# Kernel optimization log

Measured on AMD Instinct MI355X. Metric: run time of the kernel, lower is better.

Reference implementation:

```python
import jax, jax.numpy as jnp
import numpy as np

N_TOKENS = 16384
MODEL_DIM = 2048
NUM_EXPERTS = 64
K = 2


def setup_inputs() -> dict:
    key = jax.random.key(0)
    k1, k2 = jax.random.split(key)
    inputs = jax.random.normal(k1, (N_TOKENS, MODEL_DIM), dtype=jnp.float32)
    # gate weight, torch Linear(model_dim, num_experts, bias=False) -> [E, D]
    wg_weight = jax.random.normal(k2, (NUM_EXPERTS, MODEL_DIM), dtype=jnp.float32) * 0.02
    return {"inputs": inputs, "wg_weight": wg_weight}


def reference(inputs, wg_weight):
    E = wg_weight.shape[0]
    # gate computed in fp32 (module casts input and keeps wg in float32)
    logits = jnp.einsum("nd,ed->ne", inputs.astype(jnp.float32), wg_weight)
    probs = jax.nn.softmax(logits, axis=-1)                      # [N, E]
    topk_probs, topk_indices = jax.lax.top_k(probs, K)           # [N, K]
    flat_idx = topk_indices.reshape(-1)                          # [N*K]
    # stable sort of expert ids over all (token, slot) pairs
    sort_ordering = jnp.argsort(flat_idx)                        # [N*K]
    # reverse permutation: reversed[sort_ordering[i]] = i
    ar = jnp.arange(flat_idx.shape[0], dtype=sort_ordering.dtype)
    reversed_ordering = jnp.zeros_like(sort_ordering).at[sort_ordering].set(ar)
    # map slot index back to token index
    token_order = sort_ordering // K
    # per-expert counts (== unique_consecutive counts scattered into [E])
    input_splits = jnp.bincount(flat_idx, length=E).astype(jnp.int64)
    # combine weights: renormalize top-k probs via softmax when k > 1
    if K > 1:
        combine_weights = jax.nn.softmax(topk_probs, axis=-1)
    else:
        combine_weights = topk_probs
    combine_weights = combine_weights.reshape(-1).astype(inputs.dtype)
    return token_order, reversed_ordering, combine_weights, input_splits, probs
```

## Files before the change

### kernel.cpp

```cpp
#include <hip/hip_runtime.h>
#include <math.h>

#define N_TOKENS    16384
#define MODEL_DIM   2048
#define NUM_EXPERTS 64
#define NK          (N_TOKENS * 2)

#define OFF_TOKEN_ORDER 0
#define OFF_REVERSED    (NK)
#define OFF_COMBINE     (2 * NK)
#define OFF_SPLITS      (3 * NK)
#define OFF_PROBS       (3 * NK + NUM_EXPERTS)

#define NSEG 256
#define NFRAG 16384

#define B_BYTES  16384
#define A_BYTES  8192
#define STAGE_BYTES (B_BYTES + A_BYTES)

typedef _Float16 half8 __attribute__((ext_vector_type(8)));
typedef float    f32x4 __attribute__((ext_vector_type(4)));

#define MEMFENCE asm volatile("" ::: "memory")

__device__ __forceinline__ void glds16(const void* g, void* l) {
    __builtin_amdgcn_global_load_lds(
        (const __attribute__((address_space(1))) void*)g,
        (__attribute__((address_space(3))) void*)l, 16, 0, 0);
}

__global__ __launch_bounds__(256) void preconvert(
    const float* __restrict__ w, half8* __restrict__ WH, half8* __restrict__ WL,
    int* __restrict__ segHist)
{
    const int fr = blockIdx.x * 256 + threadIdx.x;
    const int lane = fr & 63;
    const int tile = (fr >> 6) & 3;
    const int kstep = fr >> 8;
    const int e = tile * 16 + (lane & 15);
    const int kb = kstep * 32 + (lane >> 4) * 8;
    const float* src = w + (size_t)e * MODEL_DIM + kb;
    const float4 w0 = *(const float4*)(src);
    const float4 w1 = *(const float4*)(src + 4);
    const float av[8] = {w0.x, w0.y, w0.z, w0.w, w1.x, w1.y, w1.z, w1.w};
    half8 hh, hl;
#pragma unroll
    for (int j = 0; j < 8; j++) {
        const float v = av[j] * 64.0f;
        const _Float16 h = (_Float16)v;
        hh[j] = h;
        hl[j] = (_Float16)((v - (float)h) * 4096.0f);
    }
    WH[fr] = hh;
    WL[fr] = hl;
    segHist[fr] = 0;
}

__global__ __launch_bounds__(256, 2) void gate_fused(
    const float* __restrict__ x, const half8* __restrict__ WH,
    const half8* __restrict__ WL, float* __restrict__ out,
    int* __restrict__ flat_idx, int* __restrict__ segHist)
{
    __shared__ alignas(16) unsigned char smem[2 * STAGE_BYTES];

    const int tid  = threadIdx.x;
    const int wv   = tid >> 6;
    const int lane = tid & 63;
    const int kh   = wv & 1;
    const int tg   = wv >> 1;
    const int t0   = blockIdx.x * 32;
    const int col  = lane & 15;
    const int kg   = lane >> 4;

    const unsigned char* s_ptr[6];
    int s_stride[6];
    int s_off[6];
#pragma unroll
    for (int i = 0; i < 6; i++) {
        const int c = wv * 6 + i;
        if (c < 16) {
            const int hl   = c & 1;
            const int tile = (c >> 1) & 3;
            const int ckh  = c >> 3;
            const half8* base = (hl ? WL : WH) + ((size_t)((ckh * 32) * 4 + tile) * 64 + lane);
            s_ptr[i]    = (const unsigned char*)base;
            s_stride[i] = 4096;
            s_off[i]    = c * 1024 + lane * 16;
        } else {
            const int a   = c - 16;
            const int cc  = a & 1;
            const int ctg = (a >> 1) & 1;
            const int ckh = a >> 2;
            const float* base = x + (size_t)(t0 + ctg * 16 + (lane & 15)) * MODEL_DIM
                              + ckh * 1024 + (lane >> 4) * 8 + cc * 4;
            s_ptr[i]    = (const unsigned char*)base;
            s_stride[i] = 128;
            s_off[i]    = B_BYTES + a * 1024 + lane * 16;
        }
    }

    f32x4 accH[4], accC[4];
    double accD[4][4];
#pragma unroll
    for (int t = 0; t < 4; t++) {
        accH[t] = (f32x4){0.f, 0.f, 0.f, 0.f};
        accC[t] = (f32x4){0.f, 0.f, 0.f, 0.f};
#pragma unroll
        for (int r = 0; r < 4; r++) accD[t][r] = 0.0;
    }

#pragma unroll
    for (int i = 0; i < 6; i++) glds16(s_ptr[i], smem + s_off[i]);

    const int aoff = B_BYTES + (kh * 4 + tg * 2) * 1024 + lane * 16;
    const int boff = (kh * 4) * 2048 + lane * 16;

    for (int j = 0; j < 32; j++) {
        const int jn = (j < 31) ? j + 1 : 31;
        unsigned char* nbuf = smem + ((j + 1) & 1) * STAGE_BYTES;
#pragma unroll
        for (int i = 0; i < 6; i++)
            glds16(s_ptr[i] + (size_t)jn * s_stride[i], nbuf + s_off[i]);

        asm volatile("s_waitcnt vmcnt(6)" ::: "memory");
        __builtin_amdgcn_s_barrier();
        MEMFENCE;

        const unsigned char* buf = smem + (j & 1) * STAGE_BYTES;

        const float4 a0 = *(const float4*)(buf + aoff);
        const float4 a1 = *(const float4*)(buf + aoff + 1024);
        const float av[8] = {a0.x, a0.y, a0.z, a0.w, a1.x, a1.y, a1.z, a1.w};
        half8 ah, al;
#pragma unroll
        for (int q = 0; q < 8; q++) {
            const float v = av[q];
            const _Float16 h = (_Float16)v;
            ah[q] = h;
            al[q] = (_Float16)((v - (float)h) * 4096.0f);
        }

#pragma unroll
        for (int t = 0; t < 4; t++) {
            const half8 bh = *(const half8*)(buf + boff + t * 2048);
            const half8 bl = *(const half8*)(buf + boff + t * 2048 + 1024);
            accH[t] = __builtin_amdgcn_mfma_f32_16x16x32_f16(ah, bh, accH[t], 0, 0, 0);
            accC[t] = __builtin_amdgcn_mfma_f32_16x16x32_f16(ah, bl, accC[t], 0, 0, 0);
            accC[t] = __builtin_amdgcn_mfma_f32_16x16x32_f16(al, bh, accC[t], 0, 0, 0);
        }

        if ((j & 7) == 7) {
#pragma unroll
            for (int t = 0; t < 4; t++)
#pragma unroll
                for (int r = 0; r < 4; r++) {
                    accD[t][r] += (double)accH[t][r] + (double)accC[t][r] * (1.0 / 4096.0);
                    accH[t][r] = 0.0f;
                    accC[t][r] = 0.0f;
                }
        }

        MEMFENCE;
        __builtin_amdgcn_s_barrier();
    }

    asm volatile("s_waitcnt vmcnt(0)" ::: "memory");
    __syncthreads();

    double* red = (double*)smem;
    if (kh == 1) {
#pragma unroll
        for (int t = 0; t < 4; t++)
#pragma unroll
            for (int r = 0; r < 4; r++)
                red[(tg * 64 + lane) * 17 + t * 4 + r] = accD[t][r];
    }
    __syncthreads();
    if (kh == 1) return;

#pragma unroll
    for (int t = 0; t < 4; t++)
#pragma unroll
        for (int r = 0; r < 4; r++)
            accD[t][r] += red[(tg * 64 + lane) * 17 + t * 4 + r];

    const int rowg = lane >> 4;
#pragma unroll
    for (int r = 0; r < 4; r++) {
        float lv[4];
#pragma unroll
        for (int t = 0; t < 4; t++) lv[t] = (float)(accD[t][r] * (1.0 / 64.0));

        float m = fmaxf(fmaxf(lv[0], lv[1]), fmaxf(lv[2], lv[3]));
#pragma unroll
        for (int d = 1; d < 16; d <<= 1) m = fmaxf(m, __shfl_xor(m, d));

        float l1 = -INFINITY, l2 = -INFINITY;
        int i1 = 0, i2 = 0;
#pragma unroll
        for (int t = 0; t < 4; t++) {
            const float l = lv[t];
            const int e = t * 16 + col;
            if (l > l1)      { l2 = l1; i2 = i1; l1 = l; i1 = e; }
            else if (l > l2) { l2 = l;  i2 = e; }
        }
#pragma unroll
        for (int d = 1; d < 16; d <<= 1) {
            const float ol1 = __shfl_xor(l1, d), ol2 = __shfl_xor(l2, d);
            const int   oi1 = __shfl_xor(i1, d), oi2 = __shfl_xor(i2, d);
            if (ol1 > l1 || (ol1 == l1 && oi1 < i1)) {
                if (l1 > ol2 || (l1 == ol2 && i1 < oi2)) { l2 = l1;  i2 = i1;  }
                else                                     { l2 = ol2; i2 = oi2; }
                l1 = ol1; i1 = oi1;
            } else if (ol1 > l2 || (ol1 == l2 && oi1 < i2)) {
                l2 = ol1; i2 = oi1;
            }
        }

        float ex[4];
        double sd = 0.0;
#pragma unroll
        for (int t = 0; t < 4; t++) { ex[t] = expf(lv[t] - m); sd += (double)ex[t]; }
#pragma unroll
        for (int d = 1; d < 16; d <<= 1) sd += __shfl_xor(sd, d);
        const float inv = (float)(1.0 / sd);

        const int tok = t0 + tg * 16 + rowg * 4 + r;
        float* pp = out + OFF_PROBS + (size_t)tok * NUM_EXPERTS + col;
#pragma unroll
        for (int t = 0; t < 4; t++) pp[t * 16] = ex[t] * inv;

        if (col == 0) {
            const float p1 = expf(l1 - m) * inv;
            const float p2 = expf(l2 - m) * inv;
            const float e2 = expf(p2 - p1);
            const float rr = 1.0f / (1.0f + e2);
            out[OFF_COMBINE + 2 * tok]     = rr;
            out[OFF_COMBINE + 2 * tok + 1] = e2 * rr;
            flat_idx[2 * tok]     = i1;
            flat_idx[2 * tok + 1] = i2;
            atomicAdd(&segHist[(tok >> 6) * NUM_EXPERTS + i1], 1);
            atomicAdd(&segHist[(tok >> 6) * NUM_EXPERTS + i2], 1);
        }
    }
}

__global__ __launch_bounds__(256) void scan_kernel(
    const int* __restrict__ segHist, int* __restrict__ segOff,
    float* __restrict__ out)
{
    __shared__ int h[NSEG * NUM_EXPERTS];
    __shared__ int gtot[4 * NUM_EXPERTS];
    __shared__ int base[NUM_EXPERTS];
    const int tid = threadIdx.x;
    for (int i = tid; i < NSEG * NUM_EXPERTS / 4; i += 256)
        *(int4*)(h + i * 4) = *(const int4*)(segHist + i * 4);
    __syncthreads();

    const int e = tid & 63;
    const int g = tid >> 6;
    int run = 0;
    for (int s = g * 64; s < g * 64 + 64; s++) {
        const int idx = s * NUM_EXPERTS + e;
        const int v = h[idx];
        h[idx] = run;
        run += v;
    }
    gtot[g * NUM_EXPERTS + e] = run;
    __syncthreads();

    if (tid < NUM_EXPERTS) {
        int b = 0;
#pragma unroll
        for (int gg = 0; gg < 4; gg++) {
            const int t = gtot[gg * NUM_EXPERTS + tid];
            gtot[gg * NUM_EXPERTS + tid] = b;
            b += t;
        }
        out[OFF_SPLITS + tid] = (float)b;
        int xs = b;
#pragma unroll
        for (int off = 1; off < 64; off <<= 1) {
            const int v = __shfl_up(xs, off);
            if (tid >= off) xs += v;
        }
        base[tid] = xs - b;
    }
    __syncthreads();

    const int myoff = gtot[g * NUM_EXPERTS + e] + base[e];
    for (int s = g * 64; s < g * 64 + 64; s++) {
        const int idx = s * NUM_EXPERTS + e;
        segOff[idx] = h[idx] + myoff;
    }
}

__global__ __launch_bounds__(256) void scatter_kernel(
    const int* __restrict__ flat_idx, const int* __restrict__ segOff,
    float* __restrict__ out)
{
    __shared__ int cnt[2 * NUM_EXPERTS];
    const int tid = threadIdx.x;
    const int i = blockIdx.x * 256 + tid;
    const int e = flat_idx[i];
    const int lane = tid & 63;
    const int wv = tid >> 6;
    const int segslot = wv >> 1;
    const int seg = i >> 7;

    if (tid < 2 * NUM_EXPERTS) cnt[tid] = 0;
    __syncthreads();

    unsigned long long match = ~0ull;
#pragma unroll
    for (int b = 0; b < 6; b++) {
        const unsigned long long m = __ballot((e >> b) & 1);
        match &= ((e >> b) & 1) ? m : ~m;
    }
    const int rank = __popcll(match & ((1ull << lane) - 1ull));

    int pos = 0;
    if ((wv & 1) == 0) {
        pos = segOff[seg * NUM_EXPERTS + e] + rank;
        if (lane == __builtin_ctzll(match))
            cnt[segslot * NUM_EXPERTS + e] = __popcll(match);
    }
    __syncthreads();
    if ((wv & 1) == 1)
        pos = segOff[seg * NUM_EXPERTS + e] + cnt[segslot * NUM_EXPERTS + e] + rank;

    out[OFF_TOKEN_ORDER + pos] = (float)(i >> 1);
    out[OFF_REVERSED + i]      = (float)pos;
}

extern "C" void kernel_launch(void* const* d_in, const int* in_sizes, int n_in,
                              void* d_out, int out_size, void* d_ws, size_t ws_size,
                              hipStream_t stream) {
    const float* x = (const float*)d_in[0];
    const float* w = (const float*)d_in[1];
    float* out = (float*)d_out;

    int* flat_idx = (int*)d_ws;
    int* segHist  = flat_idx + NK;
    int* segOff   = segHist + NSEG * NUM_EXPERTS;
    half8* WH = (half8*)(segOff + NSEG * NUM_EXPERTS);
    half8* WL = WH + NFRAG;

    preconvert<<<64, 256, 0, stream>>>(w, WH, WL, segHist);
    gate_fused<<<512, 256, 0, stream>>>(x, WH, WL, out, flat_idx, segHist);
    scan_kernel<<<1, 256, 0, stream>>>(segHist, segOff, out);
    scatter_kernel<<<NK / 256, 256, 0, stream>>>(flat_idx, segOff, out);
}
```

Baseline: 224.8 us.

## Triple-buffer global-to-LDS loads and swizzle activation tile layout

Moves the gate GEMM main loop from double to triple buffering, prefetching two stages ahead with vmcnt(12), so more global-memory latency is hidden. It also remaps which wave issues which chunk, interleaving the chunks across waves. The activation tile is reloaded with a row-per-8-lanes XOR-swizzled layout to give longer contiguous reads per token and fewer LDS bank conflicts. LDS per block grows by half, which may cut occupancy below the two blocks per CU requested.

```diff
diff --git a/kernel.cpp b/kernel.cpp
--- a/kernel.cpp
+++ b/kernel.cpp
@@ -62,7 +62,7 @@
     const half8* __restrict__ WL, float* __restrict__ out,
     int* __restrict__ flat_idx, int* __restrict__ segHist)
 {
-    __shared__ alignas(16) unsigned char smem[2 * STAGE_BYTES];
+    __shared__ alignas(16) unsigned char smem[3 * STAGE_BYTES];
 
     const int tid  = threadIdx.x;
     const int wv   = tid >> 6;
@@ -78,23 +78,23 @@
     int s_off[6];
 #pragma unroll
     for (int i = 0; i < 6; i++) {
-        const int c = wv * 6 + i;
+        const int c = i * 4 + wv;
         if (c < 16) {
             const int hl   = c & 1;
             const int tile = (c >> 1) & 3;
             const int ckh  = c >> 3;
-            const half8* base = (hl ? WL : WH) + ((size_t)((ckh * 32) * 4 + tile) * 64 + lane);
+            const half8* base = (hl ? WL : WH) + ((size_t)(ckh * 32 * 4 + tile) * 64 + lane);
             s_ptr[i]    = (const unsigned char*)base;
             s_stride[i] = 4096;
             s_off[i]    = c * 1024 + lane * 16;
         } else {
             const int a   = c - 16;
-            const int cc  = a & 1;
-            const int ctg = (a >> 1) & 1;
             const int ckh = a >> 2;
-            const float* base = x + (size_t)(t0 + ctg * 16 + (lane & 15)) * MODEL_DIM
-                              + ckh * 1024 + (lane >> 4) * 8 + cc * 4;
-            s_ptr[i]    = (const unsigned char*)base;
+            const int tgp = a & 3;
+            const int tok = t0 + tgp * 8 + (lane >> 3);
+            const int p   = (lane & 7) ^ (lane >> 3);
+            s_ptr[i]    = (const unsigned char*)(x + (size_t)tok * MODEL_DIM
+                                                 + ckh * 1024 + p * 4);
             s_stride[i] = 128;
             s_off[i]    = B_BYTES + a * 1024 + lane * 16;
         }
@@ -112,25 +112,35 @@
 
 #pragma unroll
     for (int i = 0; i < 6; i++) glds16(s_ptr[i], smem + s_off[i]);
-
-    const int aoff = B_BYTES + (kh * 4 + tg * 2) * 1024 + lane * 16;
-    const int boff = (kh * 4) * 2048 + lane * 16;
+#pragma unroll
+    for (int i = 0; i < 6; i++)
+        glds16(s_ptr[i] + s_stride[i], smem + STAGE_BYTES + s_off[i]);
+
+    const int a_r   = kh * 4 + tg * 2 + (col >> 3);
+    const int tl    = col & 7;
+    const int abase = B_BYTES + a_r * 1024 + tl * 128;
+    const int aoff0 = abase + (((kg * 2) ^ tl) << 4);
+    const int aoff1 = abase + (((kg * 2 + 1) ^ tl) << 4);
+    const int boff  = kh * 8192 + lane * 16;
+
+    int cur = 0;
+    int nxt = 2;
 
     for (int j = 0; j < 32; j++) {
-        const int jn = (j < 31) ? j + 1 : 31;
-        unsigned char* nbuf = smem + ((j + 1) & 1) * STAGE_BYTES;
+        const int jn = (j < 30) ? j + 2 : 31;
+        unsigned char* nbuf = smem + nxt * STAGE_BYTES;
 #pragma unroll
         for (int i = 0; i < 6; i++)
             glds16(s_ptr[i] + (size_t)jn * s_stride[i], nbuf + s_off[i]);
 
-        asm volatile("s_waitcnt vmcnt(6)" ::: "memory");
+        asm volatile("s_waitcnt vmcnt(12)" ::: "memory");
         __builtin_amdgcn_s_barrier();
         MEMFENCE;
 
-        const unsigned char* buf = smem + (j & 1) * STAGE_BYTES;
-
-        const float4 a0 = *(const float4*)(buf + aoff);
-        const float4 a1 = *(const float4*)(buf + aoff + 1024);
+        const unsigned char* buf = smem + cur * STAGE_BYTES;
+
+        const float4 a0 = *(const float4*)(buf + aoff0);
+        const float4 a1 = *(const float4*)(buf + aoff1);
         const float av[8] = {a0.x, a0.y, a0.z, a0.w, a1.x, a1.y, a1.z, a1.w};
         half8 ah, al;
 #pragma unroll
@@ -163,6 +173,9 @@
 
         MEMFENCE;
         __builtin_amdgcn_s_barrier();
+
+        cur = (cur == 2) ? 0 : cur + 1;
+        nxt = (nxt == 2) ? 0 : nxt + 1;
     }
 
     asm volatile("s_waitcnt vmcnt(0)" ::: "memory");
```

Result: no change. 224.2 us (-0.3%).

## Per-wave A staging with register-prefetched B and fuse scan into scatter

Applied to the files above, without the earlier changes.

The GEMM main loop drops the block-wide double-buffered LDS stage and its two barriers per step. Each wave now streams its own A tile through a swizzled triple buffer in LDS and prefetches the preconverted B fragments straight into registers, ping-ponging between two register sets. Separately, the single-block scan kernel is merged into the scatter kernel: every scatter block recomputes the full prefix scan from segHist in shared memory, which removes one launch and the segOff round trip. The cost is that the scan work is repeated in all 128 blocks, and the loop carries more register pressure.

```diff
diff --git a/kernel.cpp b/kernel.cpp
--- a/kernel.cpp
+++ b/kernel.cpp
@@ -15,14 +15,8 @@
 #define NSEG 256
 #define NFRAG 16384
 
-#define B_BYTES  16384
-#define A_BYTES  8192
-#define STAGE_BYTES (B_BYTES + A_BYTES)
-
 typedef _Float16 half8 __attribute__((ext_vector_type(8)));
 typedef float    f32x4 __attribute__((ext_vector_type(4)));
-
-#define MEMFENCE asm volatile("" ::: "memory")
 
 __device__ __forceinline__ void glds16(const void* g, void* l) {
     __builtin_amdgcn_global_load_lds(
@@ -62,7 +56,8 @@
     const half8* __restrict__ WL, float* __restrict__ out,
     int* __restrict__ flat_idx, int* __restrict__ segHist)
 {
-    __shared__ alignas(16) unsigned char smem[2 * STAGE_BYTES];
+    __shared__ alignas(16) unsigned char astage[4][3][2048];
+    __shared__ double red[128 * 17];
 
     const int tid  = threadIdx.x;
     const int wv   = tid >> 6;
@@ -73,32 +68,19 @@
     const int col  = lane & 15;
     const int kg   = lane >> 4;
 
-    const unsigned char* s_ptr[6];
-    int s_stride[6];
-    int s_off[6];
-#pragma unroll
-    for (int i = 0; i < 6; i++) {
-        const int c = wv * 6 + i;
-        if (c < 16) {
-            const int hl   = c & 1;
-            const int tile = (c >> 1) & 3;
-            const int ckh  = c >> 3;
-            const half8* base = (hl ? WL : WH) + ((size_t)((ckh * 32) * 4 + tile) * 64 + lane);
-            s_ptr[i]    = (const unsigned char*)base;
-            s_stride[i] = 4096;
-            s_off[i]    = c * 1024 + lane * 16;
-        } else {
-            const int a   = c - 16;
-            const int cc  = a & 1;
-            const int ctg = (a >> 1) & 1;
-            const int ckh = a >> 2;
-            const float* base = x + (size_t)(t0 + ctg * 16 + (lane & 15)) * MODEL_DIM
-                              + ckh * 1024 + (lane >> 4) * 8 + cc * 4;
-            s_ptr[i]    = (const unsigned char*)base;
-            s_stride[i] = 128;
-            s_off[i]    = B_BYTES + a * 1024 + lane * 16;
-        }
-    }
+    const int r3 = lane >> 3;
+    const int pp = (lane & 7) ^ r3;
+    const float* pA0 = x + (size_t)(t0 + tg * 16 + r3) * MODEL_DIM + kh * 1024 + pp * 4;
+    const float* pA1 = x + (size_t)(t0 + tg * 16 + 8 + r3) * MODEL_DIM + kh * 1024 + pp * 4;
+    unsigned char* mys = &astage[wv][0][0];
+
+    const int rr  = col & 7;
+    const int rb  = (col >> 3) * 1024 + rr * 128;
+    const int ro0 = rb + (((2 * kg)     ^ rr) << 4);
+    const int ro1 = rb + (((2 * kg + 1) ^ rr) << 4);
+
+    const half8* pbh = WH + ((size_t)kh * 32 * 4) * 64 + lane;
+    const half8* pbl = WL + ((size_t)kh * 32 * 4) * 64 + lane;
 
     f32x4 accH[4], accC[4];
     double accD[4][4];
@@ -110,65 +92,75 @@
         for (int r = 0; r < 4; r++) accD[t][r] = 0.0;
     }
 
-#pragma unroll
-    for (int i = 0; i < 6; i++) glds16(s_ptr[i], smem + s_off[i]);
-
-    const int aoff = B_BYTES + (kh * 4 + tg * 2) * 1024 + lane * 16;
-    const int boff = (kh * 4) * 2048 + lane * 16;
-
-    for (int j = 0; j < 32; j++) {
-        const int jn = (j < 31) ? j + 1 : 31;
-        unsigned char* nbuf = smem + ((j + 1) & 1) * STAGE_BYTES;
-#pragma unroll
-        for (int i = 0; i < 6; i++)
-            glds16(s_ptr[i] + (size_t)jn * s_stride[i], nbuf + s_off[i]);
-
-        asm volatile("s_waitcnt vmcnt(6)" ::: "memory");
-        __builtin_amdgcn_s_barrier();
-        MEMFENCE;
-
-        const unsigned char* buf = smem + (j & 1) * STAGE_BYTES;
-
-        const float4 a0 = *(const float4*)(buf + aoff);
-        const float4 a1 = *(const float4*)(buf + aoff + 1024);
-        const float av[8] = {a0.x, a0.y, a0.z, a0.w, a1.x, a1.y, a1.z, a1.w};
-        half8 ah, al;
-#pragma unroll
-        for (int q = 0; q < 8; q++) {
-            const float v = av[q];
-            const _Float16 h = (_Float16)v;
-            ah[q] = h;
-            al[q] = (_Float16)((v - (float)h) * 4096.0f);
-        }
-
-#pragma unroll
-        for (int t = 0; t < 4; t++) {
-            const half8 bh = *(const half8*)(buf + boff + t * 2048);
-            const half8 bl = *(const half8*)(buf + boff + t * 2048 + 1024);
-            accH[t] = __builtin_amdgcn_mfma_f32_16x16x32_f16(ah, bh, accH[t], 0, 0, 0);
-            accC[t] = __builtin_amdgcn_mfma_f32_16x16x32_f16(ah, bl, accC[t], 0, 0, 0);
-            accC[t] = __builtin_amdgcn_mfma_f32_16x16x32_f16(al, bh, accC[t], 0, 0, 0);
-        }
-
-        if ((j & 7) == 7) {
-#pragma unroll
-            for (int t = 0; t < 4; t++)
-#pragma unroll
-                for (int r = 0; r < 4; r++) {
-                    accD[t][r] += (double)accH[t][r] + (double)accC[t][r] * (1.0 / 4096.0);
-                    accH[t][r] = 0.0f;
-                    accC[t][r] = 0.0f;
-                }
-        }
-
-        MEMFENCE;
-        __builtin_amdgcn_s_barrier();
-    }
+    half8 bhA[4], blA[4], bhB[4], blB[4];
+
+    glds16(pA0, mys);
+    glds16(pA1, mys + 1024);
+    glds16(pA0 + 32, mys + 2048);
+    glds16(pA1 + 32, mys + 2048 + 1024);
+#pragma unroll
+    for (int t = 0; t < 4; t++) {
+        bhA[t] = pbh[t * 64];
+        blA[t] = pbl[t * 64];
+    }
+
+    int j = 0, curb = 0, dstb = 2;
+
+#define BODY(BHC, BLC, BHN, BLN) do {                                        \
+    const int jn2 = (j < 30) ? (j + 2) : 31;                                 \
+    glds16(pA0 + jn2 * 32, mys + dstb * 2048);                               \
+    glds16(pA1 + jn2 * 32, mys + dstb * 2048 + 1024);                        \
+    const half8* pbh_n = pbh + ((j < 31) ? 256 : 0);                         \
+    const half8* pbl_n = pbl + ((j < 31) ? 256 : 0);                         \
+    _Pragma("unroll")                                                        \
+    for (int t_ = 0; t_ < 4; t_++) {                                         \
+        BHN[t_] = pbh_n[t_ * 64];                                            \
+        BLN[t_] = pbl_n[t_ * 64];                                            \
+    }                                                                        \
+    pbh = pbh_n; pbl = pbl_n;                                                \
+    asm volatile("s_waitcnt vmcnt(10)" ::: "memory");                        \
+    __builtin_amdgcn_sched_barrier(0);                                       \
+    const float4 a0 = *(const float4*)(mys + curb * 2048 + ro0);             \
+    const float4 a1 = *(const float4*)(mys + curb * 2048 + ro1);             \
+    const float av_[8] = {a0.x, a0.y, a0.z, a0.w, a1.x, a1.y, a1.z, a1.w};   \
+    half8 ah, al;                                                            \
+    _Pragma("unroll")                                                        \
+    for (int q_ = 0; q_ < 8; q_++) {                                         \
+        const float v_ = av_[q_];                                            \
+        const _Float16 h_ = (_Float16)v_;                                    \
+        ah[q_] = h_;                                                         \
+        al[q_] = (_Float16)((v_ - (float)h_) * 4096.0f);                     \
+    }                                                                        \
+    _Pragma("unroll")                                                        \
+    for (int t_ = 0; t_ < 4; t_++) {                                         \
+        accH[t_] = __builtin_amdgcn_mfma_f32_16x16x32_f16(ah, BHC[t_], accH[t_], 0, 0, 0); \
+        accC[t_] = __builtin_amdgcn_mfma_f32_16x16x32_f16(ah, BLC[t_], accC[t_], 0, 0, 0); \
+        accC[t_] = __builtin_amdgcn_mfma_f32_16x16x32_f16(al, BHC[t_], accC[t_], 0, 0, 0); \
+    }                                                                        \
+    if ((j & 7) == 7) {                                                      \
+        _Pragma("unroll")                                                    \
+        for (int t_ = 0; t_ < 4; t_++)                                       \
+        _Pragma("unroll")                                                    \
+        for (int r_ = 0; r_ < 4; r_++) {                                     \
+            accD[t_][r_] += (double)accH[t_][r_] + (double)accC[t_][r_] * (1.0 / 4096.0); \
+            accH[t_][r_] = 0.0f;                                             \
+            accC[t_][r_] = 0.0f;                                             \
+        }                                                                    \
+    }                                                                        \
+    curb = (curb == 2) ? 0 : curb + 1;                                       \
+    dstb = (dstb == 2) ? 0 : dstb + 1;                                       \
+    j++;                                                                     \
+} while (0)
+
+    for (int jj = 0; jj < 16; jj++) {
+        BODY(bhA, blA, bhB, blB);
+        BODY(bhB, blB, bhA, blA);
+    }
+#undef BODY
 
     asm volatile("s_waitcnt vmcnt(0)" ::: "memory");
     __syncthreads();
 
-    double* red = (double*)smem;
     if (kh == 1) {
 #pragma unroll
         for (int t = 0; t < 4; t++)
@@ -227,17 +219,17 @@
         const float inv = (float)(1.0 / sd);
 
         const int tok = t0 + tg * 16 + rowg * 4 + r;
-        float* pp = out + OFF_PROBS + (size_t)tok * NUM_EXPERTS + col;
-#pragma unroll
-        for (int t = 0; t < 4; t++) pp[t * 16] = ex[t] * inv;
+        float* pp2 = out + OFF_PROBS + (size_t)tok * NUM_EXPERTS + col;
+#pragma unroll
+        for (int t = 0; t < 4; t++) pp2[t * 16] = ex[t] * inv;
 
         if (col == 0) {
             const float p1 = expf(l1 - m) * inv;
             const float p2 = expf(l2 - m) * inv;
             const float e2 = expf(p2 - p1);
-            const float rr = 1.0f / (1.0f + e2);
-            out[OFF_COMBINE + 2 * tok]     = rr;
-            out[OFF_COMBINE + 2 * tok + 1] = e2 * rr;
+            const float rr2 = 1.0f / (1.0f + e2);
+            out[OFF_COMBINE + 2 * tok]     = rr2;
+            out[OFF_COMBINE + 2 * tok + 1] = e2 * rr2;
             flat_idx[2 * tok]     = i1;
             flat_idx[2 * tok + 1] = i2;
             atomicAdd(&segHist[(tok >> 6) * NUM_EXPERTS + i1], 1);
@@ -246,16 +238,19 @@
     }
 }
 
-__global__ __launch_bounds__(256) void scan_kernel(
-    const int* __restrict__ segHist, int* __restrict__ segOff,
+__global__ __launch_bounds__(256) void scan_scatter(
+    const int* __restrict__ flat_idx, const int* __restrict__ segHist,
     float* __restrict__ out)
 {
     __shared__ int h[NSEG * NUM_EXPERTS];
     __shared__ int gtot[4 * NUM_EXPERTS];
-    __shared__ int base[NUM_EXPERTS];
+    __shared__ int base_[NUM_EXPERTS];
+    __shared__ int cnt[2 * NUM_EXPERTS];
+
     const int tid = threadIdx.x;
     for (int i = tid; i < NSEG * NUM_EXPERTS / 4; i += 256)
         *(int4*)(h + i * 4) = *(const int4*)(segHist + i * 4);
+    if (tid < 2 * NUM_EXPERTS) cnt[tid] = 0;
     __syncthreads();
 
     const int e = tid & 63;
@@ -278,57 +273,44 @@
             gtot[gg * NUM_EXPERTS + tid] = b;
             b += t;
         }
-        out[OFF_SPLITS + tid] = (float)b;
+        if (blockIdx.x == 0) out[OFF_SPLITS + tid] = (float)b;
         int xs = b;
 #pragma unroll
         for (int off = 1; off < 64; off <<= 1) {
             const int v = __shfl_up(xs, off);
             if (tid >= off) xs += v;
         }
-        base[tid] = xs - b;
-    }
-    __syncthreads();
-
-    const int myoff = gtot[g * NUM_EXPERTS + e] + base[e];
-    for (int s = g * 64; s < g * 64 + 64; s++) {
-        const int idx = s * NUM_EXPERTS + e;
-        segOff[idx] = h[idx] + myoff;
-    }
-}
-
-__global__ __launch_bounds__(256) void scatter_kernel(
-    const int* __restrict__ flat_idx, const int* __restrict__ segOff,
-    float* __restrict__ out)
-{
-    __shared__ int cnt[2 * NUM_EXPERTS];
-    const int tid = threadIdx.x;
+        base_[tid] = xs - b;
+    }
+    __syncthreads();
+
     const int i = blockIdx.x * 256 + tid;
-    const int e = flat_idx[i];
+    const int ee = flat_idx[i];
     const int lane = tid & 63;
     const int wv = tid >> 6;
     const int segslot = wv >> 1;
     const int seg = i >> 7;
 
-    if (tid < 2 * NUM_EXPERTS) cnt[tid] = 0;
-    __syncthreads();
-
     unsigned long long match = ~0ull;
 #pragma unroll
     for (int b = 0; b < 6; b++) {
-        const unsigned long long m = __ballot((e >> b) & 1);
-        match &= ((e >> b) & 1) ? m : ~m;
+        const unsigned long long m = __ballot((ee >> b) & 1);
+        match &= ((ee >> b) & 1) ? m : ~m;
     }
     const int rank = __popcll(match & ((1ull << lane) - 1ull));
+
+    const int segoff = h[seg * NUM_EXPERTS + ee]
+                     + gtot[(seg >> 6) * NUM_EXPERTS + ee] + base_[ee];
 
     int pos = 0;
     if ((wv & 1) == 0) {
-        pos = segOff[seg * NUM_EXPERTS + e] + rank;
+        pos = segoff + rank;
         if (lane == __builtin_ctzll(match))
-            cnt[segslot * NUM_EXPERTS + e] = __popcll(match);
+            cnt[segslot * NUM_EXPERTS + ee] = __popcll(match);
     }
     __syncthreads();
     if ((wv & 1) == 1)
-        pos = segOff[seg * NUM_EXPERTS + e] + cnt[segslot * NUM_EXPERTS + e] + rank;
+        pos = segoff + cnt[segslot * NUM_EXPERTS + ee] + rank;
 
     out[OFF_TOKEN_ORDER + pos] = (float)(i >> 1);
     out[OFF_REVERSED + i]      = (float)pos;
@@ -343,12 +325,10 @@
 
     int* flat_idx = (int*)d_ws;
     int* segHist  = flat_idx + NK;
-    int* segOff   = segHist + NSEG * NUM_EXPERTS;
-    half8* WH = (half8*)(segOff + NSEG * NUM_EXPERTS);
+    half8* WH = (half8*)(segHist + NSEG * NUM_EXPERTS);
     half8* WL = WH + NFRAG;
 
     preconvert<<<64, 256, 0, stream>>>(w, WH, WL, segHist);
     gate_fused<<<512, 256, 0, stream>>>(x, WH, WL, out, flat_idx, segHist);
-    scan_kernel<<<1, 256, 0, stream>>>(segHist, segOff, out);
-    scatter_kernel<<<NK / 256, 256, 0, stream>>>(flat_idx, segOff, out);
-}
+    scan_scatter<<<NK / 256, 256, 0, stream>>>(flat_idx, segHist, out);
+}
```

After: 226.2 us. Within noise of the previous version (+0.6%).
